# Kernel optimization log

Measured on AMD Instinct MI355X. Metric: run time of the kernel, lower is better.

Reference implementation:

```python
import jax, jax.numpy as jnp
import numpy as np

N_POINTS = 131072
NUM_FREQS = 6
MIN_LOG2_FREQ = 0.0
MAX_LOG2_FREQ = 5.0
NUM_QUANTS = 80
NUM_FEATS = 4
NUM_CORRS = 8
STD = 1e-4


def setup_inputs() -> dict:
    key = jax.random.key(0)
    k1, k2 = jax.random.split(key)
    # points in [-1, 1] as typical normalized NeRF scene coordinates
    points = jax.random.uniform(k1, (N_POINTS, 3), jnp.float32, -1.0, 1.0)
    # QFF1.__init__: std ** (1/x_dim), qff_vector ~ randn * std'
    std = STD ** (1.0 / 3.0)
    qff_vector = jax.random.normal(
        k2, (NUM_FREQS * 2 * 3, NUM_FEATS * NUM_CORRS, NUM_QUANTS, 1), jnp.float32) * std
    freqs = (2.0 ** jnp.linspace(MIN_LOG2_FREQ, MAX_LOG2_FREQ, NUM_FREQS)).astype(jnp.float32)
    return {"points": points, "qff_vector": qff_vector, "freqs": freqs}


def _lerp_lookup(qv, enc):
    # 1D linear interpolation, equivalent to F.grid_sample(bilinear, align_corners=True)
    # on a (Q, 1) grid with x coord fixed to 0.
    # qv: (M, CR, Q) tables; enc: (M, N) coords in [-1, 1].
    Q = qv.shape[-1]
    pos = (enc + 1.0) * 0.5 * (Q - 1)            # (M, N) in [0, Q-1]
    i0 = jnp.clip(jnp.floor(pos), 0, Q - 1).astype(jnp.int32)
    i1 = jnp.minimum(i0 + 1, Q - 1)
    w = (pos - i0.astype(pos.dtype))[:, None, :]  # (M, 1, N)
    gather = jax.vmap(lambda q, i: q[:, i])       # per-row gather: (CR, Q), (N) -> (CR, N)
    v0 = gather(qv, i0)                           # (M, CR, N)
    v1 = gather(qv, i1)
    return v0 * (1.0 - w) + v1 * w


def reference(points, qff_vector, freqs):
    # points: (N, 3); qff_vector: (NF*2*3, C*R, Q, 1); freqs: (NF,)
    N = points.shape[0]
    NF = freqs.shape[0]
    CR, Q = qff_vector.shape[1], qff_vector.shape[2]
    R = NUM_CORRS
    C = CR // R
    # pos_encode: (NF, 3, N) -> stack sin/cos -> (NF*2*3, N)
    fp = points.T[None, :, :] * freqs[:, None, None]
    enc = jnp.stack((jnp.sin(fp), jnp.cos(fp)), 1).reshape(NF * 2 * 3, N)
    qv = qff_vector.reshape(NF * 2 * 3, CR, Q)
    sampled = _lerp_lookup(qv, enc)               # (NF*2*3, C*R, N)
    sampled = sampled.reshape(NF * 2, 3, C, R, N)
    # CP decomposition: product over the 3 axes, sum over rank R
    f = (sampled[:, 0] * sampled[:, 1] * sampled[:, 2]).sum(2)  # (NF*2, C, N)
    return f.reshape(NF * 2 * C, N).T             # (N, latent_dim=NF*2*C)
```

## Files before the change

### kernel.cpp

```cpp
#include <hip/hip_runtime.h>
#include <hip/hip_fp16.h>
#include <math.h>


constexpr int N_POINTS = 131072;
constexpr int NFREQ    = 6;
constexpr int QN       = 80;
constexpr int CRN      = 32;
constexpr int M_PER_F  = 6;
constexpr int ROW      = 40;
constexpr int MSTRIDE  = QN * ROW;
constexpr int TSTRIDE  = CRN * QN;
constexpr int FH       = M_PER_F * MSTRIDE;
constexpr int FH4      = FH / 8;
constexpr int NTAB     = NFREQ * M_PER_F;
constexpr int TB       = 1024;
constexpr int PPB      = 512;
constexpr int NBLK     = N_POINTS / PPB;
constexpr int DSTR     = 25;
constexpr size_t TAB_BYTES = (size_t)NTAB * MSTRIDE * 2;

typedef float f32x4 __attribute__((ext_vector_type(4)));

__global__ __launch_bounds__(256)
void qff1_prep(const float* __restrict__ qff, __half* __restrict__ wsh)
{
    int i = blockIdx.x * 256 + threadIdx.x;
    if (i >= NTAB * TSTRIDE) return;
    int T  = i / TSTRIDE;
    int r  = i - T * TSTRIDE;
    int cr = r / QN;
    int q  = r - cr * QN;
    wsh[T * MSTRIDE + q * ROW + cr] = __float2half(qff[i]);
}

__global__ __launch_bounds__(TB, 4)
void qff1_main(const float* __restrict__ points,
               const __half* __restrict__ wsh,
               const float* __restrict__ freqs,
               float4* __restrict__ out4)
{
    __shared__ __align__(16) __half  tabA[FH];
    __shared__ __align__(16) __half  tabB[FH];
    __shared__ __align__(16) __half2 dmp2[PPB * DSTR];

    const int tid = threadIdx.x;
    const int p   = tid & (PPB - 1);
    const int h   = tid >> 9;
    const int n   = blockIdx.x * PPB + p;

    const float px = points[n * 3 + 0];
    const float py = points[n * 3 + 1];
    const float pz = points[n * 3 + 2];

    const int i0 = tid, i1 = tid + TB, i2 = tid + 2 * TB;

    {
        const float4* src = reinterpret_cast<const float4*>(wsh);
        float4* dst = reinterpret_cast<float4*>(tabA);
        dst[i0] = src[i0];
        dst[i1] = src[i1];
        if (i2 < FH4) dst[i2] = src[i2];
    }
    __syncthreads();

    for (int f = 0; f < NFREQ; ++f) {
        const __half* cur = (f & 1) ? tabB : tabA;
        float4* nxt = reinterpret_cast<float4*>((f & 1) ? tabA : tabB);
        const bool more = (f + 1 < NFREQ);

        float4 sv0, sv1, sv2;
        if (more) {
            const float4* src =
                reinterpret_cast<const float4*>(wsh + (size_t)(f + 1) * FH);
            sv0 = src[i0];
            sv1 = src[i1];
            if (i2 < FH4) sv2 = src[i2];
        }

        const float freq = freqs[f];
        float ee[3];
        {
            float s0, c0, s1, c1, s2, c2;
            __sincosf(px * freq, &s0, &c0);
            __sincosf(py * freq, &s1, &c1);
            __sincosf(pz * freq, &s2, &c2);
            ee[0] = h ? c0 : s0;
            ee[1] = h ? c1 : s1;
            ee[2] = h ? c2 : s2;
        }

        int b0[3], b1[3];
        __half2 w2[3];
#pragma unroll
        for (int d = 0; d < 3; ++d) {
            float pos = (ee[d] + 1.0f) * (0.5f * (float)(QN - 1));
            float fi  = floorf(pos);
            int q0    = (int)fi;
            q0 = q0 < 0 ? 0 : (q0 > QN - 1 ? QN - 1 : q0);
            int q1 = q0 + 1; if (q1 > QN - 1) q1 = QN - 1;
            w2[d] = __float2half2_rn(pos - (float)q0);
            int m = h * 3 + d;
            b0[d] = m * MSTRIDE + q0 * ROW;
            b1[d] = m * MSTRIDE + q1 * ROW;
        }

        float acc[4];
#pragma unroll
        for (int jc = 0; jc < 4; ++jc) {
            __half2 Lv[3][4];
#pragma unroll
            for (int d = 0; d < 3; ++d) {
                union { float4 v; __half2 hh[4]; } A, B;
                A.v = *(const float4*)&cur[b0[d] + jc * 8];
                B.v = *(const float4*)&cur[b1[d] + jc * 8];
#pragma unroll
                for (int kk = 0; kk < 4; ++kk)
                    Lv[d][kk] = __hfma2(w2[d], __hsub2(B.hh[kk], A.hh[kk]), A.hh[kk]);
            }
            float a = 0.0f;
#pragma unroll
            for (int kk = 0; kk < 4; ++kk) {
                float2 f0 = __half22float2(Lv[0][kk]);
                float2 f1 = __half22float2(Lv[1][kk]);
                float2 f2 = __half22float2(Lv[2][kk]);
                a += f0.x * f1.x * f2.x + f0.y * f1.y * f2.y;
            }
            acc[jc] = a;
        }

        dmp2[p * DSTR + h * 12 + f * 2 + 0] = __floats2half2_rn(acc[0], acc[1]);
        dmp2[p * DSTR + h * 12 + f * 2 + 1] = __floats2half2_rn(acc[2], acc[3]);

        if (more) {
            nxt[i0] = sv0;
            nxt[i1] = sv1;
            if (i2 < FH4) nxt[i2] = sv2;
        }
        __syncthreads();
    }

    const size_t base = (size_t)blockIdx.x * (PPB * 12);
#pragma unroll
    for (int k = 0; k < 6; ++k) {
        int i  = tid + k * TB;
        int pp = i / 12;
        int c  = i - pp * 12;
        int off = (c & 1) * 12 + (c >> 1) * 2;
        float2 lo = __half22float2(dmp2[pp * DSTR + off + 0]);
        float2 hi = __half22float2(dmp2[pp * DSTR + off + 1]);
        f32x4 v = { lo.x, lo.y, hi.x, hi.y };
        __builtin_nontemporal_store(v, (f32x4*)&out4[base + i]);
    }
}

__global__ __launch_bounds__(512, 8)
void qff1_fallback(const float* __restrict__ points,
                   const float* __restrict__ qff,
                   const float* __restrict__ freqs,
                   float* __restrict__ out)
{
    __shared__ __align__(16) __half tab[FH];
    const int tid = threadIdx.x;
    const int f   = blockIdx.y;

    const float* tsrc = qff + (size_t)f * (M_PER_F * CRN * QN);
    __half2* lds2 = reinterpret_cast<__half2*>(tab);
    for (int idx = tid; idx < M_PER_F * QN * (CRN / 2); idx += 512) {
        int m   = idx / (QN * CRN / 2);
        int rem = idx - m * (QN * CRN / 2);
        int q   = rem >> 4;
        int cr2 = rem & 15;
        float v0 = tsrc[m * (CRN * QN) + (2 * cr2    ) * QN + q];
        float v1 = tsrc[m * (CRN * QN) + (2 * cr2 + 1) * QN + q];
        lds2[m * (MSTRIDE / 2) + q * (ROW / 2) + cr2] = __floats2half2_rn(v0, v1);
    }
    __syncthreads();

    const int n = blockIdx.x * 512 + tid;
    const float px = points[n * 3 + 0];
    const float py = points[n * 3 + 1];
    const float pz = points[n * 3 + 2];
    const float freq = freqs[f];

    float enc[6];
    {
        float s, cc;
        __sincosf(px * freq, &s, &cc); enc[0] = s; enc[3] = cc;
        __sincosf(py * freq, &s, &cc); enc[1] = s; enc[4] = cc;
        __sincosf(pz * freq, &s, &cc); enc[2] = s; enc[5] = cc;
    }
    int b0[6], b1[6];
    __half2 w2[6];
#pragma unroll
    for (int m = 0; m < 6; ++m) {
        float pos = (enc[m] + 1.0f) * (0.5f * (float)(QN - 1));
        float fi  = floorf(pos);
        int q0    = (int)fi;
        q0 = q0 < 0 ? 0 : (q0 > QN - 1 ? QN - 1 : q0);
        int q1 = q0 + 1; if (q1 > QN - 1) q1 = QN - 1;
        w2[m] = __float2half2_rn(pos - (float)q0);
        b0[m] = m * MSTRIDE + q0 * ROW;
        b1[m] = m * MSTRIDE + q1 * ROW;
    }
    float accv[8];
#pragma unroll
    for (int s = 0; s < 2; ++s) {
#pragma unroll
        for (int jc = 0; jc < 4; ++jc) {
            __half2 Lv[3][4];
#pragma unroll
            for (int d = 0; d < 3; ++d) {
                int m = s * 3 + d;
                union { float4 v; __half2 hh[4]; } A, B;
                A.v = *(const float4*)&tab[b0[m] + jc * 8];
                B.v = *(const float4*)&tab[b1[m] + jc * 8];
#pragma unroll
                for (int kk = 0; kk < 4; ++kk)
                    Lv[d][kk] = __hfma2(w2[m], __hsub2(B.hh[kk], A.hh[kk]), A.hh[kk]);
            }
            float a = 0.0f;
#pragma unroll
            for (int kk = 0; kk < 4; ++kk) {
                float2 f0 = __half22float2(Lv[0][kk]);
                float2 f1 = __half22float2(Lv[1][kk]);
                float2 f2 = __half22float2(Lv[2][kk]);
                a += f0.x * f1.x * f2.x + f0.y * f1.y * f2.y;
            }
            accv[s * 4 + jc] = a;
        }
    }
    float4* o = (float4*)(out + (size_t)n * 48 + f * 8);
    o[0] = make_float4(accv[0], accv[1], accv[2], accv[3]);
    o[1] = make_float4(accv[4], accv[5], accv[6], accv[7]);
}

extern "C" void kernel_launch(void* const* d_in, const int* in_sizes, int n_in,
                              void* d_out, int out_size, void* d_ws, size_t ws_size,
                              hipStream_t stream) {
    const float* points = (const float*)d_in[0];
    const float* qff    = (const float*)d_in[1];
    const float* freqs  = (const float*)d_in[2];
    float* out = (float*)d_out;

    if (ws_size >= TAB_BYTES) {
        __half* wsh = (__half*)d_ws;
        qff1_prep<<<dim3((NTAB * TSTRIDE + 255) / 256), dim3(256), 0, stream>>>(qff, wsh);
        qff1_main<<<dim3(NBLK), dim3(TB), 0, stream>>>(points, wsh, freqs, (float4*)out);
    } else {
        qff1_fallback<<<dim3(N_POINTS / 512, NFREQ), dim3(512), 0, stream>>>(points, qff, freqs, out);
    }
}
```

Baseline: 32.34 us.

## Halve block size and single-buffer the LDS table to raise occupancy

Cuts the main kernel to 512 threads handling 256 points per block and replaces the double-buffered LDS table with one buffer. The next frequency's table is still prefetched into registers, but it is written only after an added barrier, so each frequency now costs two barriers. Sin/cos is now evaluated only for the half each thread needs instead of a full sincos. The aim is lower LDS use per block so more blocks fit per CU. The price is more register staging per thread (five float4), twice as many blocks each reloading the table, and less overlap between table loads and compute.

```diff
diff --git a/kernel.cpp b/kernel.cpp
--- a/kernel.cpp
+++ b/kernel.cpp
@@ -14,8 +14,8 @@
 constexpr int FH       = M_PER_F * MSTRIDE;
 constexpr int FH4      = FH / 8;
 constexpr int NTAB     = NFREQ * M_PER_F;
-constexpr int TB       = 1024;
-constexpr int PPB      = 512;
+constexpr int TB       = 512;
+constexpr int PPB      = 256;
 constexpr int NBLK     = N_POINTS / PPB;
 constexpr int DSTR     = 25;
 constexpr size_t TAB_BYTES = (size_t)NTAB * MSTRIDE * 2;
@@ -40,58 +40,57 @@
                const float* __restrict__ freqs,
                float4* __restrict__ out4)
 {
-    __shared__ __align__(16) __half  tabA[FH];
-    __shared__ __align__(16) __half  tabB[FH];
+    __shared__ __align__(16) __half  tab[FH];
     __shared__ __align__(16) __half2 dmp2[PPB * DSTR];
 
     const int tid = threadIdx.x;
     const int p   = tid & (PPB - 1);
-    const int h   = tid >> 9;
+    const int h   = tid >> 8;
     const int n   = blockIdx.x * PPB + p;
 
     const float px = points[n * 3 + 0];
     const float py = points[n * 3 + 1];
     const float pz = points[n * 3 + 2];
 
-    const int i0 = tid, i1 = tid + TB, i2 = tid + 2 * TB;
+    const int i4 = tid + 4 * TB;
 
     {
         const float4* src = reinterpret_cast<const float4*>(wsh);
-        float4* dst = reinterpret_cast<float4*>(tabA);
-        dst[i0] = src[i0];
-        dst[i1] = src[i1];
-        if (i2 < FH4) dst[i2] = src[i2];
+        float4* dst = reinterpret_cast<float4*>(tab);
+        dst[tid]          = src[tid];
+        dst[tid + TB]     = src[tid + TB];
+        dst[tid + 2 * TB] = src[tid + 2 * TB];
+        dst[tid + 3 * TB] = src[tid + 3 * TB];
+        if (i4 < FH4) dst[i4] = src[i4];
     }
     __syncthreads();
 
     for (int f = 0; f < NFREQ; ++f) {
-        const __half* cur = (f & 1) ? tabB : tabA;
-        float4* nxt = reinterpret_cast<float4*>((f & 1) ? tabA : tabB);
         const bool more = (f + 1 < NFREQ);
 
-        float4 sv0, sv1, sv2;
+        float4 sv0, sv1, sv2, sv3, sv4;
         if (more) {
             const float4* src =
                 reinterpret_cast<const float4*>(wsh + (size_t)(f + 1) * FH);
-            sv0 = src[i0];
-            sv1 = src[i1];
-            if (i2 < FH4) sv2 = src[i2];
+            sv0 = src[tid];
+            sv1 = src[tid + TB];
+            sv2 = src[tid + 2 * TB];
+            sv3 = src[tid + 3 * TB];
+            if (i4 < FH4) sv4 = src[i4];
         }
 
         const float freq = freqs[f];
-        float ee[3];
-        {
-            float s0, c0, s1, c1, s2, c2;
-            __sincosf(px * freq, &s0, &c0);
-            __sincosf(py * freq, &s1, &c1);
-            __sincosf(pz * freq, &s2, &c2);
-            ee[0] = h ? c0 : s0;
-            ee[1] = h ? c1 : s1;
-            ee[2] = h ? c2 : s2;
+
+        float e0, e1, e2;
+        if (h == 0) {
+            e0 = __sinf(px * freq); e1 = __sinf(py * freq); e2 = __sinf(pz * freq);
+        } else {
+            e0 = __cosf(px * freq); e1 = __cosf(py * freq); e2 = __cosf(pz * freq);
         }
 
         int b0[3], b1[3];
         __half2 w2[3];
+        float ee[3] = { e0, e1, e2 };
 #pragma unroll
         for (int d = 0; d < 3; ++d) {
             float pos = (ee[d] + 1.0f) * (0.5f * (float)(QN - 1));
@@ -112,8 +111,8 @@
 #pragma unroll
             for (int d = 0; d < 3; ++d) {
                 union { float4 v; __half2 hh[4]; } A, B;
-                A.v = *(const float4*)&cur[b0[d] + jc * 8];
-                B.v = *(const float4*)&cur[b1[d] + jc * 8];
+                A.v = *(const float4*)&tab[b0[d] + jc * 8];
+                B.v = *(const float4*)&tab[b1[d] + jc * 8];
 #pragma unroll
                 for (int kk = 0; kk < 4; ++kk)
                     Lv[d][kk] = __hfma2(w2[d], __hsub2(B.hh[kk], A.hh[kk]), A.hh[kk]);
@@ -132,12 +131,17 @@
         dmp2[p * DSTR + h * 12 + f * 2 + 0] = __floats2half2_rn(acc[0], acc[1]);
         dmp2[p * DSTR + h * 12 + f * 2 + 1] = __floats2half2_rn(acc[2], acc[3]);
 
+        __syncthreads();
+
         if (more) {
-            nxt[i0] = sv0;
-            nxt[i1] = sv1;
-            if (i2 < FH4) nxt[i2] = sv2;
-        }
-        __syncthreads();
+            float4* dst = reinterpret_cast<float4*>(tab);
+            dst[tid]          = sv0;
+            dst[tid + TB]     = sv1;
+            dst[tid + 2 * TB] = sv2;
+            dst[tid + 3 * TB] = sv3;
+            if (i4 < FH4) dst[i4] = sv4;
+            __syncthreads();
+        }
     }
 
     const size_t base = (size_t)blockIdx.x * (PPB * 12);
```

Measured after the change: 33.33 us. 1.03x slower.
